# Kernel optimization log

Measured on AMD Instinct MI355X. Metric: run time of the kernel, lower is better.

Reference implementation:

```python
import jax, jax.numpy as jnp
import numpy as np

B, S, D, H = 2, 2048, 1024, 16
DH = D // H

def setup_inputs() -> dict:
    key = jax.random.key(0)
    ks = jax.random.split(key, 5)
    sd = 0.02
    return {
        'x': jax.random.normal(ks[0], (B, S, D), dtype=jnp.float32),
        'Wq': jax.random.normal(ks[1], (D, D), dtype=jnp.float32) * sd,
        'Wk': jax.random.normal(ks[2], (D, D), dtype=jnp.float32) * sd,
        'Wv': jax.random.normal(ks[3], (D, D), dtype=jnp.float32) * sd,
        'Wo': jax.random.normal(ks[4], (D, D), dtype=jnp.float32) * sd,
        'bo': jnp.zeros((D,), dtype=jnp.float32),
    }

def reference(x, Wq, Wk, Wv, Wo, bo):
    b, s, _ = x.shape
    scale = DH ** -0.5
    def split_heads(t):
        return t.reshape(b, s, H, DH).transpose(0, 2, 1, 3)  # (b, h, s, dh)
    q = split_heads(x @ Wq.T)
    k = split_heads(x @ Wk.T)
    v = split_heads(x @ Wv.T)
    scores = jnp.einsum('bhqd,bhkd->bhqk', q, k)
    causal = jnp.triu(jnp.ones((s, s), dtype=bool), k=1)
    scores = jnp.where(causal, -jnp.inf, scores)
    attn = jax.nn.softmax(scores * scale, axis=-1)  # dropout p=0 -> identity (x2)
    ctx = jnp.einsum('bhqk,bhkd->bhqd', attn, v)
    ctx = ctx.transpose(0, 2, 1, 3).reshape(b, s, D)
    return ctx @ Wo.T + bo
```

## Files before the change

### kernel.cpp

```cpp
#include <hip/hip_runtime.h>
#include <hip/hip_bf16.h>


constexpr int Bc = 2, Sc = 2048, Dc = 1024, Hc = 16, DHc = 64;

typedef __attribute__((ext_vector_type(8))) short short8;
typedef __attribute__((ext_vector_type(4))) float floatx4;
typedef __attribute__((ext_vector_type(4))) unsigned short ushort4v;

#define MFMA16(a, b, c) __builtin_amdgcn_mfma_f32_16x16x32_bf16((a), (b), (c), 0, 0, 0)

#if __has_builtin(__builtin_amdgcn_exp2f)
#define EXP2F(x) __builtin_amdgcn_exp2f(x)
#else
#define EXP2F(x) __expf((x) * 0.6931471805599453f)
#endif

__device__ __forceinline__ unsigned short f2bf(float f) {
    union { float f; unsigned u; } v; v.f = f;
    unsigned u = v.u + 0x7fffu + ((v.u >> 16) & 1u);
    return (unsigned short)(u >> 16);
}

__device__ __forceinline__ unsigned short f2bf_trunc(float f) {
    union { float f; unsigned u; } v; v.f = f;
    return (unsigned short)(v.u >> 16);
}

__device__ __forceinline__ short8 pack8(const float4& a, const float4& b) {
    short8 r;
    r[0] = (short)f2bf(a.x); r[1] = (short)f2bf(a.y);
    r[2] = (short)f2bf(a.z); r[3] = (short)f2bf(a.w);
    r[4] = (short)f2bf(b.x); r[5] = (short)f2bf(b.y);
    r[6] = (short)f2bf(b.z); r[7] = (short)f2bf(b.w);
    return r;
}

__device__ __forceinline__ void async16(const unsigned short* g, unsigned short* l) {
    __builtin_amdgcn_global_load_lds(
        (const __attribute__((address_space(1))) void*)g,
        (__attribute__((address_space(3))) void*)l, 16, 0, 0);
}

__global__ __launch_bounds__(256) void to_bf16(
    const float* __restrict__ x,  const float* __restrict__ Wq,
    const float* __restrict__ Wk, const float* __restrict__ Wv,
    const float* __restrict__ Wo,
    unsigned short* __restrict__ xb,  unsigned short* __restrict__ Wqb,
    unsigned short* __restrict__ Wkb, unsigned short* __restrict__ Wvb,
    unsigned short* __restrict__ Wob)
{
    const size_t base = ((size_t)blockIdx.x * 256 + threadIdx.x) * 8;
    const float* s; unsigned short* d; size_t off;
    if (base < 4194304) { s = x; d = xb; off = base; }
    else {
        size_t r = base - 4194304;
        int seg = (int)(r >> 20);
        off = r & 1048575;
        s = seg == 0 ? Wq : seg == 1 ? Wk : seg == 2 ? Wv : Wo;
        d = seg == 0 ? Wqb : seg == 1 ? Wkb : seg == 2 ? Wvb : Wob;
    }
    const float4 a = *(const float4*)(s + off);
    const float4 b = *(const float4*)(s + off + 4);
    *(short8*)(d + off) = pack8(a, b);
}

__global__ __launch_bounds__(256) void qkv_gemm(
    const unsigned short* __restrict__ A,
    const unsigned short* __restrict__ Wqb, const unsigned short* __restrict__ Wkb,
    const unsigned short* __restrict__ Wvb,
    unsigned short* __restrict__ Qo, unsigned short* __restrict__ Ko,
    unsigned short* __restrict__ Vt)
{
    __shared__ unsigned short As[2][128 * 32];
    __shared__ unsigned short Bs[2][128 * 32];
    const int which = blockIdx.z;
    const unsigned short* __restrict__ W =
        which == 0 ? Wqb : (which == 1 ? Wkb : Wvb);
    const int m0 = blockIdx.y * 128, n0 = blockIdx.x * 128;
    const int tid = threadIdx.x, wv = tid >> 6, lane = tid & 63;
    const int quad = lane >> 4, l16 = lane & 15;
    const int qm = wv >> 1, qn = wv & 1;
    const int srow = tid >> 2, sch = tid & 3;

    floatx4 acc[4][4];
    #pragma unroll
    for (int i = 0; i < 4; ++i)
        #pragma unroll
        for (int j = 0; j < 4; ++j) acc[i][j] = floatx4{0.f, 0.f, 0.f, 0.f};

    auto stage = [&](int bufi, int k0) {
        #pragma unroll
        for (int cl = 0; cl < 2; ++cl) {
            const int row = cl * 64 + srow;
            const int col = ((sch ^ (row & 3)) << 3);
            async16(A + (size_t)(m0 + row) * Dc + k0 + col,
                    &As[bufi][cl * 2048 + wv * 512]);
            async16(W + (size_t)(n0 + row) * Dc + k0 + col,
                    &Bs[bufi][cl * 2048 + wv * 512]);
        }
    };

    int buf = 0;
    stage(0, 0);
    for (int k0 = 0; k0 < Dc; k0 += 32) {
        __syncthreads();
        if (k0 + 32 < Dc) stage(buf ^ 1, k0 + 32);
        short8 af[4], bfv[4];
        #pragma unroll
        for (int i = 0; i < 4; ++i) {
            const int row = qm * 64 + i * 16 + l16;
            af[i] = *(const short8*)&As[buf][row * 32 + ((quad ^ (l16 & 3)) << 3)];
        }
        #pragma unroll
        for (int j = 0; j < 4; ++j) {
            const int row = qn * 64 + j * 16 + l16;
            bfv[j] = *(const short8*)&Bs[buf][row * 32 + ((quad ^ (l16 & 3)) << 3)];
        }
        #pragma unroll
        for (int i = 0; i < 4; ++i)
            #pragma unroll
            for (int j = 0; j < 4; ++j)
                acc[i][j] = MFMA16(af[i], bfv[j], acc[i][j]);
        buf ^= 1;
    }

    const int h = blockIdx.x * 2 + qn;
    #pragma unroll
    for (int i = 0; i < 4; ++i) {
        const int mrow = m0 + qm * 64 + i * 16 + quad * 4;
        const int b = mrow >> 11;
        const int sb = mrow & (Sc - 1);
        #pragma unroll
        for (int j = 0; j < 4; ++j) {
            const int dh = j * 16 + l16;
            if (which == 2) {
                ushort4v pk;
                pk[0] = f2bf(acc[i][j][0]); pk[1] = f2bf(acc[i][j][1]);
                pk[2] = f2bf(acc[i][j][2]); pk[3] = f2bf(acc[i][j][3]);
                *(ushort4v*)&Vt[(size_t)((b * Hc + h) * DHc + dh) * Sc + sb] = pk;
            } else {
                unsigned short* __restrict__ O = which ? Ko : Qo;
                #pragma unroll
                for (int r = 0; r < 4; ++r)
                    O[(size_t)((b * Hc + h) * Sc + sb + r) * DHc + dh] =
                        f2bf(acc[i][j][r]);
            }
        }
    }
}

__global__ __launch_bounds__(256) void attn(
    const unsigned short* __restrict__ Q,
    const unsigned short* __restrict__ K,
    const unsigned short* __restrict__ Vt,
    unsigned short* __restrict__ ctx)
{
    __shared__ unsigned short Ks[2][64 * 64];
    __shared__ unsigned short Vs[2][64 * 64];
    __shared__ unsigned short Pl[4][16][40];
    const int bh = blockIdx.x;
    const int y  = (int)blockIdx.y;
    const int qt = (y < 16) ? (31 - y) : (y - 16);
    const int tid = threadIdx.x, wv = tid >> 6, lane = tid & 63;
    const int quad = lane >> 4, l16 = lane & 15;
    const int b = bh >> 4, h = bh & 15;
    const float c1 = 0.125f * 1.44269504f;
    const float c2 = -3.0f  * 1.44269504f;
    const floatx4 zero4 = {0.f, 0.f, 0.f, 0.f};

    const int qbase = qt * 64 + wv * 16;

    const unsigned short* Kb = K  + (size_t)bh * Sc * DHc;
    const unsigned short* Vb = Vt + (size_t)bh * DHc * Sc;
    const int sr = tid >> 3, sc8 = tid & 7;
    const int chA = ((quad       ^ (l16 & 7)) << 3);
    const int chB = (((4 + quad) ^ (l16 & 7)) << 3);

    const unsigned short* Qp = Q + (size_t)(bh * Sc + qbase + l16) * DHc;
    const short8 qf0 = *(const short8*)(Qp + quad * 8);
    const short8 qf1 = *(const short8*)(Qp + 32 + quad * 8);

    floatx4 o[4];
    #pragma unroll
    for (int j = 0; j < 4; ++j) o[j] = zero4;
    float lsum[4] = {0.f, 0.f, 0.f, 0.f};

    auto stageKV = [&](int bufi, int k0) {
        #pragma unroll
        for (int cl = 0; cl < 2; ++cl) {
            const int row = cl * 32 + sr;
            const int col = ((sc8 ^ (row & 7)) << 3);
            async16(Kb + (size_t)(k0 + row) * DHc + col,
                    &Ks[bufi][cl * 2048 + wv * 512]);
            async16(Vb + (size_t)row * Sc + k0 + col,
                    &Vs[bufi][cl * 2048 + wv * 512]);
        }
    };

    int buf = 0;
    stageKV(0, 0);
    for (int t = 0; t <= qt; ++t) {
        __syncthreads();
        if (t < qt) stageKV(buf ^ 1, (t + 1) * 64);
        const int k0 = t * 64;
        const bool diag = (t == qt);

        floatx4 sc4[4];
        #pragma unroll
        for (int s = 0; s < 4; ++s) {
            const int row = s * 16 + l16;
            const short8 kf0 = *(const short8*)&Ks[buf][row * 64 + chA];
            const short8 kf1 = *(const short8*)&Ks[buf][row * 64 + chB];
            floatx4 tt = MFMA16(qf0, kf0, zero4);
            sc4[s] = MFMA16(qf1, kf1, tt);
        }
        #pragma unroll
        for (int hf = 0; hf < 2; ++hf) {
            #pragma unroll
            for (int s2 = 0; s2 < 2; ++s2) {
                const int s = hf * 2 + s2;
                const int key = k0 + s * 16 + l16;
                #pragma unroll
                for (int r = 0; r < 4; ++r) {
                    float e = EXP2F(fmaf(sc4[s][r], c1, c2));
                    if (diag) {
                        const int qrow = qbase + quad * 4 + r;
                        e = (key > qrow) ? 0.f : e;
                    }
                    lsum[r] += e;
                    Pl[wv][quad * 4 + r][s2 * 16 + l16] = f2bf_trunc(e);
                }
            }
            const short8 pf = *(const short8*)&Pl[wv][l16][quad * 8];
            const int ch = hf ? chB : chA;
            #pragma unroll
            for (int j = 0; j < 4; ++j) {
                const int row = j * 16 + l16;
                const short8 vf = *(const short8*)&Vs[buf][row * 64 + ch];
                o[j] = MFMA16(pf, vf, o[j]);
            }
        }
        buf ^= 1;
    }

    #pragma unroll
    for (int r = 0; r < 4; ++r) {
        float ls = lsum[r];
        #pragma unroll
        for (int off = 1; off < 16; off <<= 1)
            ls += __shfl_xor(ls, off);
        lsum[r] = ls;
    }
    #pragma unroll
    for (int r = 0; r < 4; ++r) {
        const int q = qbase + quad * 4 + r;
        const float inv = 1.f / lsum[r];
        unsigned short* cp = ctx + (size_t)(b * Sc + q) * Dc + h * DHc + l16;
        #pragma unroll
        for (int j = 0; j < 4; ++j)
            cp[j * 16] = f2bf(o[j][r] * inv);
    }
}

__global__ __launch_bounds__(256) void out_gemm(
    const unsigned short* __restrict__ A,
    const unsigned short* __restrict__ Wob,
    const float* __restrict__ bo,
    float* __restrict__ out)
{
    __shared__ unsigned short As[2][128 * 32];
    __shared__ unsigned short Bs[2][64 * 32];
    const int m0 = blockIdx.y * 128, n0 = blockIdx.x * 64;
    const int tid = threadIdx.x, wv = tid >> 6, lane = tid & 63;
    const int quad = lane >> 4, l16 = lane & 15;
    const int srow = tid >> 2, sch = tid & 3;

    floatx4 acc[2][4];
    #pragma unroll
    for (int i = 0; i < 2; ++i)
        #pragma unroll
        for (int j = 0; j < 4; ++j) acc[i][j] = floatx4{0.f, 0.f, 0.f, 0.f};

    auto stage = [&](int bufi, int k0) {
        #pragma unroll
        for (int cl = 0; cl < 2; ++cl) {
            const int row = cl * 64 + srow;
            const int col = ((sch ^ (row & 3)) << 3);
            async16(A + (size_t)(m0 + row) * Dc + k0 + col,
                    &As[bufi][cl * 2048 + wv * 512]);
        }
        const int col = ((sch ^ (srow & 3)) << 3);
        async16(Wob + (size_t)(n0 + srow) * Dc + k0 + col,
                &Bs[bufi][wv * 512]);
    };

    int buf = 0;
    stage(0, 0);
    for (int k0 = 0; k0 < Dc; k0 += 32) {
        __syncthreads();
        if (k0 + 32 < Dc) stage(buf ^ 1, k0 + 32);
        short8 af[2], bfv[4];
        #pragma unroll
        for (int i = 0; i < 2; ++i) {
            const int row = wv * 32 + i * 16 + l16;
            af[i] = *(const short8*)&As[buf][row * 32 + ((quad ^ (l16 & 3)) << 3)];
        }
        #pragma unroll
        for (int j = 0; j < 4; ++j) {
            const int row = j * 16 + l16;
            bfv[j] = *(const short8*)&Bs[buf][row * 32 + ((quad ^ (l16 & 3)) << 3)];
        }
        #pragma unroll
        for (int i = 0; i < 2; ++i)
            #pragma unroll
            for (int j = 0; j < 4; ++j)
                acc[i][j] = MFMA16(af[i], bfv[j], acc[i][j]);
        buf ^= 1;
    }

    #pragma unroll
    for (int i = 0; i < 2; ++i) {
        const int m = m0 + wv * 32 + i * 16 + quad * 4;
        #pragma unroll
        for (int j = 0; j < 4; ++j) {
            const int n = n0 + j * 16 + l16;
            const float bias = bo[n];
            #pragma unroll
            for (int r = 0; r < 4; ++r)
                out[(size_t)(m + r) * Dc + n] = acc[i][j][r] + bias;
        }
    }
}

extern "C" void kernel_launch(void* const* d_in, const int* in_sizes, int n_in,
                              void* d_out, int out_size, void* d_ws, size_t ws_size,
                              hipStream_t stream) {
    const float* x  = (const float*)d_in[0];
    const float* Wq = (const float*)d_in[1];
    const float* Wk = (const float*)d_in[2];
    const float* Wv = (const float*)d_in[3];
    const float* Wo = (const float*)d_in[4];
    const float* bo = (const float*)d_in[5];
    float* out = (float*)d_out;

    const size_t xel = (size_t)Bc * Sc * Dc;
    const size_t wel = (size_t)Dc * Dc;
    unsigned short* xb  = (unsigned short*)d_ws;
    unsigned short* Wqb = xb  + xel;
    unsigned short* Wkb = Wqb + wel;
    unsigned short* Wvb = Wkb + wel;
    unsigned short* Wob = Wvb + wel;
    unsigned short* Qb  = Wob + wel;
    unsigned short* Kb  = Qb  + xel;
    unsigned short* Vtb = Kb  + xel;
    unsigned short* cx  = Vtb + xel;

    to_bf16<<<dim3((xel + 4 * wel) / (256 * 8)), 256, 0, stream>>>(
        x, Wq, Wk, Wv, Wo, xb, Wqb, Wkb, Wvb, Wob);
    qkv_gemm<<<dim3(Dc / 128, (Bc * Sc) / 128, 3), 256, 0, stream>>>(
        xb, Wqb, Wkb, Wvb, Qb, Kb, Vtb);
    attn<<<dim3(Bc * Hc, 32), 256, 0, stream>>>(Qb, Kb, Vtb, cx);
    out_gemm<<<dim3(Dc / 64, (Bc * Sc) / 128), 256, 0, stream>>>(cx, Wob, bo, out);
}
```

Before: 180.8 us.

## Process 128-query tiles per attention block so each K/V tile is reused twice

Each attention block now handles 128 query rows, with every wave owning two 16-row query fragments, instead of 64 rows. Every staged K/V tile in shared memory therefore feeds twice as many MFMAs, halving K/V global loads and barriers per query, and the grid shrinks to 16 blocks along y. Per-fragment activity and mask flags skip MFMAs above the causal diagonal. The cost is twice the accumulator registers per wave, which may lower occupancy, and only 512 blocks, with a remapped tile order meant to balance the causal work.

```diff
diff --git a/kernel.cpp b/kernel.cpp
--- a/kernel.cpp
+++ b/kernel.cpp
@@ -158,10 +158,11 @@
 {
     __shared__ unsigned short Ks[2][64 * 64];
     __shared__ unsigned short Vs[2][64 * 64];
-    __shared__ unsigned short Pl[4][16][40];
+    __shared__ unsigned short Pl[4][2][16][40];
     const int bh = blockIdx.x;
     const int y  = (int)blockIdx.y;
-    const int qt = (y < 16) ? (31 - y) : (y - 16);
+    const int p  = (y < 8) ? y : 23 - y;
+    const int Tmax = 2 * p + 1;
     const int tid = threadIdx.x, wv = tid >> 6, lane = tid & 63;
     const int quad = lane >> 4, l16 = lane & 15;
     const int b = bh >> 4, h = bh & 15;
@@ -169,7 +170,9 @@
     const float c2 = -3.0f  * 1.44269504f;
     const floatx4 zero4 = {0.f, 0.f, 0.f, 0.f};
 
-    const int qbase = qt * 64 + wv * 16;
+    int qb[2];
+    qb[0] = 128 * p + 32 * wv;
+    qb[1] = qb[0] + 16;
 
     const unsigned short* Kb = K  + (size_t)bh * Sc * DHc;
     const unsigned short* Vb = Vt + (size_t)bh * DHc * Sc;
@@ -177,14 +180,23 @@
     const int chA = ((quad       ^ (l16 & 7)) << 3);
     const int chB = (((4 + quad) ^ (l16 & 7)) << 3);
 
-    const unsigned short* Qp = Q + (size_t)(bh * Sc + qbase + l16) * DHc;
-    const short8 qf0 = *(const short8*)(Qp + quad * 8);
-    const short8 qf1 = *(const short8*)(Qp + 32 + quad * 8);
-
-    floatx4 o[4];
-    #pragma unroll
-    for (int j = 0; j < 4; ++j) o[j] = zero4;
-    float lsum[4] = {0.f, 0.f, 0.f, 0.f};
+    short8 qf[2][2];
+    #pragma unroll
+    for (int m = 0; m < 2; ++m) {
+        const unsigned short* Qp = Q + (size_t)(bh * Sc + qb[m] + l16) * DHc;
+        qf[m][0] = *(const short8*)(Qp + quad * 8);
+        qf[m][1] = *(const short8*)(Qp + 32 + quad * 8);
+    }
+
+    floatx4 o[2][4];
+    float lsum[2][4];
+    #pragma unroll
+    for (int m = 0; m < 2; ++m)
+        #pragma unroll
+        for (int j = 0; j < 4; ++j) {
+            o[m][j] = zero4;
+            lsum[m][j] = 0.f;
+        }
 
     auto stageKV = [&](int bufi, int k0) {
         #pragma unroll
@@ -200,66 +212,87 @@
 
     int buf = 0;
     stageKV(0, 0);
-    for (int t = 0; t <= qt; ++t) {
+    for (int t = 0; t <= Tmax; ++t) {
         __syncthreads();
-        if (t < qt) stageKV(buf ^ 1, (t + 1) * 64);
+        if (t < Tmax) stageKV(buf ^ 1, (t + 1) * 64);
         const int k0 = t * 64;
-        const bool diag = (t == qt);
-
-        floatx4 sc4[4];
+        bool act[2], msk[2];
+        #pragma unroll
+        for (int m = 0; m < 2; ++m) {
+            act[m] = (k0 <= qb[m] + 15);
+            msk[m] = (k0 + 63 > qb[m]);
+        }
+
+        floatx4 sc4[2][4];
         #pragma unroll
         for (int s = 0; s < 4; ++s) {
             const int row = s * 16 + l16;
             const short8 kf0 = *(const short8*)&Ks[buf][row * 64 + chA];
             const short8 kf1 = *(const short8*)&Ks[buf][row * 64 + chB];
-            floatx4 tt = MFMA16(qf0, kf0, zero4);
-            sc4[s] = MFMA16(qf1, kf1, tt);
+            #pragma unroll
+            for (int m = 0; m < 2; ++m)
+                if (act[m]) {
+                    floatx4 tt = MFMA16(qf[m][0], kf0, zero4);
+                    sc4[m][s] = MFMA16(qf[m][1], kf1, tt);
+                }
         }
         #pragma unroll
         for (int hf = 0; hf < 2; ++hf) {
             #pragma unroll
-            for (int s2 = 0; s2 < 2; ++s2) {
-                const int s = hf * 2 + s2;
-                const int key = k0 + s * 16 + l16;
-                #pragma unroll
-                for (int r = 0; r < 4; ++r) {
-                    float e = EXP2F(fmaf(sc4[s][r], c1, c2));
-                    if (diag) {
-                        const int qrow = qbase + quad * 4 + r;
-                        e = (key > qrow) ? 0.f : e;
+            for (int m = 0; m < 2; ++m)
+                if (act[m]) {
+                    #pragma unroll
+                    for (int s2 = 0; s2 < 2; ++s2) {
+                        const int s = hf * 2 + s2;
+                        const int key = k0 + s * 16 + l16;
+                        #pragma unroll
+                        for (int r = 0; r < 4; ++r) {
+                            float e = EXP2F(fmaf(sc4[m][s][r], c1, c2));
+                            if (msk[m]) {
+                                const int qrow = qb[m] + quad * 4 + r;
+                                e = (key > qrow) ? 0.f : e;
+                            }
+                            lsum[m][r] += e;
+                            Pl[wv][m][quad * 4 + r][s2 * 16 + l16] = f2bf_trunc(e);
+                        }
                     }
-                    lsum[r] += e;
-                    Pl[wv][quad * 4 + r][s2 * 16 + l16] = f2bf_trunc(e);
                 }
-            }
-            const short8 pf = *(const short8*)&Pl[wv][l16][quad * 8];
+            short8 pf[2];
+            #pragma unroll
+            for (int m = 0; m < 2; ++m)
+                if (act[m]) pf[m] = *(const short8*)&Pl[wv][m][l16][quad * 8];
             const int ch = hf ? chB : chA;
             #pragma unroll
             for (int j = 0; j < 4; ++j) {
                 const int row = j * 16 + l16;
                 const short8 vf = *(const short8*)&Vs[buf][row * 64 + ch];
-                o[j] = MFMA16(pf, vf, o[j]);
+                #pragma unroll
+                for (int m = 0; m < 2; ++m)
+                    if (act[m]) o[m][j] = MFMA16(pf[m], vf, o[m][j]);
             }
         }
         buf ^= 1;
     }
 
     #pragma unroll
-    for (int r = 0; r < 4; ++r) {
-        float ls = lsum[r];
-        #pragma unroll
-        for (int off = 1; off < 16; off <<= 1)
-            ls += __shfl_xor(ls, off);
-        lsum[r] = ls;
-    }
-    #pragma unroll
-    for (int r = 0; r < 4; ++r) {
-        const int q = qbase + quad * 4 + r;
-        const float inv = 1.f / lsum[r];
-        unsigned short* cp = ctx + (size_t)(b * Sc + q) * Dc + h * DHc + l16;
-        #pragma unroll
-        for (int j = 0; j < 4; ++j)
-            cp[j * 16] = f2bf(o[j][r] * inv);
+    for (int m = 0; m < 2; ++m) {
+        #pragma unroll
+        for (int r = 0; r < 4; ++r) {
+            float ls = lsum[m][r];
+            #pragma unroll
+            for (int off = 1; off < 16; off <<= 1)
+                ls += __shfl_xor(ls, off);
+            lsum[m][r] = ls;
+        }
+        #pragma unroll
+        for (int r = 0; r < 4; ++r) {
+            const int q = qb[m] + quad * 4 + r;
+            const float inv = 1.f / lsum[m][r];
+            unsigned short* cp = ctx + (size_t)(b * Sc + q) * Dc + h * DHc + l16;
+            #pragma unroll
+            for (int j = 0; j < 4; ++j)
+                cp[j * 16] = f2bf(o[m][j][r] * inv);
+        }
     }
 }
 
@@ -360,6 +393,6 @@
         x, Wq, Wk, Wv, Wo, xb, Wqb, Wkb, Wvb, Wob);
     qkv_gemm<<<dim3(Dc / 128, (Bc * Sc) / 128, 3), 256, 0, stream>>>(
         xb, Wqb, Wkb, Wvb, Qb, Kb, Vtb);
-    attn<<<dim3(Bc * Hc, 32), 256, 0, stream>>>(Qb, Kb, Vtb, cx);
+    attn<<<dim3(Bc * Hc, 16), 256, 0, stream>>>(Qb, Kb, Vtb, cx);
     out_gemm<<<dim3(Dc / 64, (Bc * Sc) / 128), 256, 0, stream>>>(cx, Wob, bo, out);
 }
```

New measurement: 213.9 us. 1.18x slower.
